# Kernel tuning notes

Hardware: AMD Instinct MI355X
Metric: run time of the kernel (lower is better)

Reference implementation:

```python
import jax, jax.numpy as jnp
import numpy as np

C = 64          # channels
HEADS = 4       # num_heads -> head_dim = 16
HID = int(C * 2.66)  # 170, GDFN hidden channels
B, H, W = 2, 256, 256


def conv1x1(x, w):
    # x: (b,c,h,w), w: (o,c) -> pointwise conv, no bias
    return jnp.einsum('bchw,oc->bohw', x, w)


def dwconv3x3(x, w):
    # depthwise 3x3, SAME padding; w: (C,1,3,3)
    return jax.lax.conv_general_dilated(
        x, w, window_strides=(1, 1), padding='SAME',
        feature_group_count=x.shape[1],
        dimension_numbers=('NCHW', 'OIHW', 'NCHW'))


def layer_norm_c(x, w, b):
    # torch: LayerNorm over channel dim of (b, hw, c), eps=1e-5
    mu = x.mean(axis=1, keepdims=True)
    var = ((x - mu) ** 2).mean(axis=1, keepdims=True)
    xn = (x - mu) / jnp.sqrt(var + 1e-5)
    return xn * w[None, :, None, None] + b[None, :, None, None]


def l2norm(x):
    # F.normalize(dim=-1), eps=1e-12
    n = jnp.sqrt(jnp.sum(x * x, axis=-1, keepdims=True))
    return x / jnp.maximum(n, 1e-12)


def mdta(x, temp, w_qkv, w_qkv_dw, w_po, w_kv, w_kv_dw, w_pof):
    b, c, h, w_ = x.shape
    d = c // HEADS
    qkv = dwconv3x3(conv1x1(x, w_qkv), w_qkv_dw)
    q, k, v = jnp.split(qkv, 3, axis=1)
    rs = lambda t: t.reshape(b, HEADS, d, h * w_)
    q, k, v = l2norm(rs(q)), l2norm(rs(k)), rs(v)
    # channel attention: (b,heads,d,d), softmax over last dim
    attn = jax.nn.softmax(jnp.einsum('bhdn,bhen->bhde', q, k) * temp, axis=-1)
    out = conv1x1(jnp.einsum('bhde,bhen->bhdn', attn, v).reshape(b, c, h, w_), w_po)
    # second gated branch: kv from `out`, reuse attn (qf/kf/attnf are dead code in source)
    kvf = dwconv3x3(conv1x1(out, w_kv), w_kv_dw)
    _kf, vf = jnp.split(kvf, 2, axis=1)
    vf = rs(vf)
    outf = conv1x1(jnp.einsum('bhde,bhen->bhdn', attn, vf).reshape(b, c, h, w_), w_pof)
    return outf


def gdfn(x, w_in, w_dw, w_out):
    x12 = dwconv3x3(conv1x1(x, w_in), w_dw)
    x1, x2 = jnp.split(x12, 2, axis=1)
    return conv1x1(jax.nn.gelu(x1, approximate=False) * x2, w_out)


def setup_inputs() -> dict:
    key = jax.random.key(0)
    ks = jax.random.split(key, 10)
    s = 0.05
    return {
        'x': jax.random.normal(ks[0], (B, C, H, W), jnp.float32),
        'n1_w': jnp.ones((C,), jnp.float32),
        'n1_b': jnp.zeros((C,), jnp.float32),
        'temp': jnp.ones((1, HEADS, 1, 1), jnp.float32),
        'w_qkv': jax.random.normal(ks[1], (3 * C, C), jnp.float32) * s,
        'w_qkv_dw': jax.random.normal(ks[2], (3 * C, 1, 3, 3), jnp.float32) * s,
        'w_po': jax.random.normal(ks[3], (C, C), jnp.float32) * s,
        'w_kv': jax.random.normal(ks[4], (2 * C, C), jnp.float32) * s,
        'w_kv_dw': jax.random.normal(ks[5], (2 * C, 1, 3, 3), jnp.float32) * s,
        'w_pof': jax.random.normal(ks[6], (C, C), jnp.float32) * s,
        'n2_w': jnp.ones((C,), jnp.float32),
        'n2_b': jnp.zeros((C,), jnp.float32),
        'w_in': jax.random.normal(ks[7], (2 * HID, C), jnp.float32) * s,
        'w_dw': jax.random.normal(ks[8], (2 * HID, 1, 3, 3), jnp.float32) * s,
        'w_out': jax.random.normal(ks[9], (C, HID), jnp.float32) * s,
    }


def reference(x, n1_w, n1_b, temp, w_qkv, w_qkv_dw, w_po, w_kv, w_kv_dw, w_pof,
              n2_w, n2_b, w_in, w_dw, w_out):
    x = x + mdta(layer_norm_c(x, n1_w, n1_b), temp,
                 w_qkv, w_qkv_dw, w_po, w_kv, w_kv_dw, w_pof)
    x = x + gdfn(layer_norm_c(x, n2_w, n2_b), w_in, w_dw, w_out)
    return x
```

## Files before the change

### kernel.cpp

```cpp
#include <hip/hip_runtime.h>
#include <hip/hip_bf16.h>
#include <math.h>

#define NPB 65536
#define BATCH 2
#define NTOT (BATCH * NPB)

typedef unsigned short u16;
typedef __attribute__((ext_vector_type(8))) short short8;
typedef __attribute__((ext_vector_type(4))) short short4v;
typedef __attribute__((ext_vector_type(4))) float f32x4;


__device__ __forceinline__ float bf2f(u16 u) {
  union { unsigned u; float f; } v; v.u = ((unsigned)u) << 16; return v.f;
}
__device__ __forceinline__ u16 f2bf(float f) {
  union { float f; unsigned u; } v; v.f = f;
  unsigned r = v.u + 0x7FFFu + ((v.u >> 16) & 1u);
  return (u16)(r >> 16);
}
__device__ __forceinline__ unsigned pk2(float a, float b) {
  return (unsigned)f2bf(a) | ((unsigned)f2bf(b) << 16);
}
__device__ __forceinline__ f32x4 mm(short8 a, short8 b, f32x4 c) {
  return __builtin_amdgcn_mfma_f32_16x16x32_bf16(a, b, c, 0, 0, 0);
}
__device__ __forceinline__ short8 ldfrag(const u16* F, int frag, int l) {
  return *reinterpret_cast<const short8*>(F + ((size_t)frag * 64 + l) * 8);
}
__device__ __forceinline__ void st4(u16* p, f32x4 c) {
  uint2 v; v.x = pk2(c[0], c[1]); v.y = pk2(c[2], c[3]);
  *reinterpret_cast<uint2*>(p) = v;
}
__device__ __forceinline__ float gelu_t(float a) {
  const float z = 0.7978845608f * fmaf(0.044715f * a, a * a, a);
  const float e = __expf(2.f * z);
  const float th = 1.f - 2.f / (e + 1.f);
  return 0.5f * a * (1.f + th);
}

__global__ __launch_bounds__(64) void k_wprep(
    const float* __restrict__ wqkv, const float* __restrict__ win,
    const float* __restrict__ wout, u16* __restrict__ WQf,
    u16* __restrict__ WIf, u16* __restrict__ WOf)
{
  const int f = blockIdx.x;
  const int l = threadIdx.x;
  const int fr = l & 15, fq = l >> 4;
  short8 v;
  u16* dst;
  if (f < 24) {
    const int t = f >> 1, kh = f & 1;
    const int row = t * 16 + fr;
#pragma unroll
    for (int j = 0; j < 8; ++j)
      v[j] = (short)f2bf(wqkv[(size_t)row * 64 + kh * 32 + fq * 8 + j]);
    dst = WQf + ((size_t)f * 64 + l) * 8;
  } else if (f < 68) {
    const int fi = f - 24;
    const int g = fi >> 1, kh = fi & 1;
    const int half = g / 11, t = g % 11;
    const int col = half * 176 + t * 16 + fr;
    const int row = col < 170 ? col : (col < 176 ? -1 : (col < 346 ? col - 6 : -1));
#pragma unroll
    for (int j = 0; j < 8; ++j)
      v[j] = (row < 0) ? (short)0
             : (short)f2bf(win[(size_t)row * 64 + kh * 32 + fq * 8 + j]);
    dst = WIf + ((size_t)fi * 64 + l) * 8;
  } else {
    const int fi = f - 68;
    const int t = fi / 6, kh = fi % 6;
    const int row = t * 16 + fr;
#pragma unroll
    for (int j = 0; j < 8; ++j) {
      const int k = kh * 32 + fq * 8 + j;
      v[j] = (k < 170) ? (short)f2bf(wout[(size_t)row * 170 + k]) : (short)0;
    }
    dst = WOf + ((size_t)fi * 64 + l) * 8;
  }
  *reinterpret_cast<short8*>(dst) = v;
}

__global__ __launch_bounds__(256, 4) void k_ln1(
    const float* __restrict__ x, const float* __restrict__ n1w,
    const float* __restrict__ n1b, u16* __restrict__ Y1)
{
  const int n = blockIdx.x * 256 + threadIdx.x;
  const int b = blockIdx.y;
  const size_t pix = (size_t)b * NPB + n;
  const float* xb = x + ((size_t)b * 64) * NPB + n;
  float y[64];
  float mu = 0.f;
#pragma unroll
  for (int c = 0; c < 64; ++c) { y[c] = xb[(size_t)c * NPB]; mu += y[c]; }
  mu *= (1.f / 64.f);
  float var = 0.f;
#pragma unroll
  for (int c = 0; c < 64; ++c) { float d = y[c] - mu; var = fmaf(d, d, var); }
  const float rstd = rsqrtf(var * (1.f / 64.f) + 1e-5f);
#pragma unroll
  for (int c = 0; c < 64; ++c) y[c] = (y[c] - mu) * rstd * n1w[c] + n1b[c];
#pragma unroll
  for (int cb = 0; cb < 4; ++cb) {
    u16* dst = Y1 + ((size_t)cb * NTOT + pix) * 16;
    uint4 v0, v1;
    v0.x = pk2(y[cb*16+0],  y[cb*16+1]);  v0.y = pk2(y[cb*16+2],  y[cb*16+3]);
    v0.z = pk2(y[cb*16+4],  y[cb*16+5]);  v0.w = pk2(y[cb*16+6],  y[cb*16+7]);
    v1.x = pk2(y[cb*16+8],  y[cb*16+9]);  v1.y = pk2(y[cb*16+10], y[cb*16+11]);
    v1.z = pk2(y[cb*16+12], y[cb*16+13]); v1.w = pk2(y[cb*16+14], y[cb*16+15]);
    *reinterpret_cast<uint4*>(dst) = v0;
    *reinterpret_cast<uint4*>(dst + 8) = v1;
  }
}

__global__ __launch_bounds__(256, 2) void g_qkvp(
    const u16* __restrict__ Y1, const u16* __restrict__ WQf,
    u16* __restrict__ qkvp)
{
  const int l = threadIdx.x & 63, fr = l & 15, fq = l >> 4;
  const int wv = blockIdx.x * 4 + (threadIdx.x >> 6);
  const int nw = gridDim.x * 4;
  short8 A[12][2];
#pragma unroll
  for (int t = 0; t < 12; ++t)
#pragma unroll
    for (int kh = 0; kh < 2; ++kh) A[t][kh] = ldfrag(WQf, t * 2 + kh, l);
  const size_t hof = (size_t)(fq & 1) * 8;
  for (int tile = wv; tile < 8192; tile += nw) {
    const size_t n = (size_t)tile * 16 + fr;
    const short8 b0 = *reinterpret_cast<const short8*>(
        Y1 + (((size_t)(fq >> 1)) * NTOT + n) * 16 + hof);
    const short8 b1 = *reinterpret_cast<const short8*>(
        Y1 + (((size_t)(2 + (fq >> 1))) * NTOT + n) * 16 + hof);
    f32x4 c[12];
#pragma unroll
    for (int t = 0; t < 12; ++t) c[t] = f32x4{0.f, 0.f, 0.f, 0.f};
#pragma unroll
    for (int t = 0; t < 12; ++t) c[t] = mm(A[t][0], b0, c[t]);
#pragma unroll
    for (int t = 0; t < 12; ++t) c[t] = mm(A[t][1], b1, c[t]);
#pragma unroll
    for (int t = 0; t < 12; ++t)
      st4(qkvp + ((size_t)t * NTOT + n) * 16 + fq * 4, c[t]);
  }
}

template<int CH, int STRIP>
__global__ __launch_bounds__(256, 2) void k_dwr(
    const u16* __restrict__ in, u16* __restrict__ out,
    const float* __restrict__ wdw, int wofs)
{
  typedef short __attribute__((ext_vector_type(CH))) shortC;
  constexpr int LPP = 16 / CH;
  constexpr int NX  = 256 / LPP;
  constexpr int XC  = 256 / NX;
  const int t = threadIdx.x;
  const int sub = t % LPP, xi = t / LPP;
  const int q = blockIdx.x / XC, xc = blockIdx.x % XC;
  const int strip = blockIdx.y, b = blockIdx.z;
  const int x = xc * NX + xi;
  const int y0 = strip * STRIP;
  const int e0 = sub * CH;
  const int c0 = q * 16 + e0;

  const u16* pin = in + ((size_t)q * NTOT + (size_t)b * NPB) * 16 + e0;

  float w[9][CH];
#pragma unroll
  for (int ch = 0; ch < CH; ++ch) {
    const int row = wofs + c0 + ch;
#pragma unroll
    for (int tap = 0; tap < 9; ++tap)
      w[tap][ch] = wdw[(size_t)row * 9 + tap];
  }

  auto LD = [&](int yy, int xx) -> shortC {
    shortC v;
#pragma unroll
    for (int j = 0; j < CH; ++j) v[j] = 0;
    if ((unsigned)yy < 256u && (unsigned)xx < 256u)
      v = *reinterpret_cast<const shortC*>(pin + (size_t)(yy * 256 + xx) * 16);
    return v;
  };

  shortC r[3][3];
  r[0][0] = LD(y0 - 1, x - 1); r[0][1] = LD(y0 - 1, x); r[0][2] = LD(y0 - 1, x + 1);
  r[1][0] = LD(y0, x - 1);     r[1][1] = LD(y0, x);     r[1][2] = LD(y0, x + 1);

#pragma unroll 2
  for (int yy = 0; yy < STRIP; ++yy) {
    const int y = y0 + yy;
    r[2][0] = LD(y + 1, x - 1); r[2][1] = LD(y + 1, x); r[2][2] = LD(y + 1, x + 1);
    float acc[CH];
#pragma unroll
    for (int ch = 0; ch < CH; ++ch) acc[ch] = 0.f;
#pragma unroll
    for (int ky = 0; ky < 3; ++ky)
#pragma unroll
      for (int kx = 0; kx < 3; ++kx)
#pragma unroll
        for (int ch = 0; ch < CH; ++ch)
          acc[ch] = fmaf(w[ky * 3 + kx][ch], bf2f((u16)r[ky][kx][ch]), acc[ch]);
    u16* po = out + ((size_t)q * NTOT + (size_t)b * NPB +
                     (size_t)(y * 256 + x)) * 16 + e0;
    uint4 o;
    o.x = pk2(acc[0], acc[1]); o.y = pk2(acc[2], acc[3]);
    o.z = pk2(acc[4], acc[5]); o.w = pk2(acc[6], acc[7]);
    *reinterpret_cast<uint4*>(po) = o;
#pragma unroll
    for (int dx = 0; dx < 3; ++dx) { r[0][dx] = r[1][dx]; r[1][dx] = r[2][dx]; }
  }
}

__global__ __launch_bounds__(256, 2) void g_windwg(
    const u16* __restrict__ Y2, const u16* __restrict__ WIf,
    const float* __restrict__ wdw, u16* __restrict__ Hg)
{
  __shared__ __align__(16) u16 sy[336 * 72];
  __shared__ __align__(16) u16 sh[336 * 36];
  __shared__ __align__(16) u16 swt[2 * 9 * 176];
  const int t = threadIdx.x;
  const int tx0 = blockIdx.x * 16, ty0 = blockIdx.y * 16;
  const int b = blockIdx.z;
  const size_t bofs = (size_t)b * NPB;

  for (int i = t; i < 2 * 9 * 176; i += 256) {
    const int pl = i / (9 * 176);
    const int r = i % (9 * 176);
    const int tap = r / 176, c = r % 176;
    swt[i] = (c < 170) ? f2bf(wdw[((size_t)(pl * 170 + c)) * 9 + tap]) : (u16)0;
  }
  for (int idx = t; idx < 336; idx += 256) {
    const int py = idx / 18, px = idx % 18;
    const int gy = ty0 + py - 1, gx = tx0 + px - 1;
    const bool ok = (idx < 324) && ((unsigned)gy < 256u) && ((unsigned)gx < 256u);
#pragma unroll
    for (int cb = 0; cb < 4; ++cb) {
      short8 v0, v1;
      if (ok) {
        const u16* src = Y2 + ((size_t)cb * NTOT + bofs + (size_t)(gy * 256 + gx)) * 16;
        v0 = *reinterpret_cast<const short8*>(src);
        v1 = *reinterpret_cast<const short8*>(src + 8);
      } else {
#pragma unroll
        for (int j = 0; j < 8; ++j) { v0[j] = 0; v1[j] = 0; }
      }
      *reinterpret_cast<short8*>(&sy[idx * 72 + cb * 16]) = v0;
      *reinterpret_cast<short8*>(&sy[idx * 72 + cb * 16 + 8]) = v1;
    }
  }
  __syncthreads();

  const int w = t >> 6, l = t & 63, fr = l & 15, fq = l >> 4;
  const int sub = t & 3, colx = (t >> 2) & 15, rg = t >> 6;
  const int e0 = sub * 4;

  for (int q = 0; q < 11; ++q) {
    const short8 a10 = ldfrag(WIf, q * 2, l);
    const short8 a11 = ldfrag(WIf, q * 2 + 1, l);
    const short8 a20 = ldfrag(WIf, (11 + q) * 2, l);
    const short8 a21 = ldfrag(WIf, (11 + q) * 2 + 1, l);
    for (int i = w; i < 21; i += 4) {
      const u16* sp = &sy[(i * 16 + fr) * 72];
      const short8 b0 = *reinterpret_cast<const short8*>(sp + fq * 8);
      const short8 b1 = *reinterpret_cast<const short8*>(sp + 32 + fq * 8);
      f32x4 c1 = {0.f, 0.f, 0.f, 0.f}, c2 = {0.f, 0.f, 0.f, 0.f};
      c1 = mm(a10, b0, c1); c1 = mm(a11, b1, c1);
      c2 = mm(a20, b0, c2); c2 = mm(a21, b1, c2);
      u16* dp = &sh[(i * 16 + fr) * 36];
      st4(dp + fq * 4, c1);
      st4(dp + 16 + fq * 4, c2);
    }
    __syncthreads();

    float wf[2][9][4];
#pragma unroll
    for (int pl = 0; pl < 2; ++pl)
#pragma unroll
      for (int tap = 0; tap < 9; ++tap) {
        const short4v wv = *reinterpret_cast<const short4v*>(
            &swt[(pl * 9 + tap) * 176 + q * 16 + e0]);
#pragma unroll
        for (int j = 0; j < 4; ++j) wf[pl][tap][j] = bf2f((u16)wv[j]);
      }
    short4v rwin[3][3][2];
    auto LDR = [&](int hr, int slot) {
#pragma unroll
      for (int dx = 0; dx < 3; ++dx)
#pragma unroll
        for (int pl = 0; pl < 2; ++pl)
          rwin[slot][dx][pl] = *reinterpret_cast<const short4v*>(
              &sh[(hr * 18 + colx + dx) * 36 + pl * 16 + e0]);
    };
    const int r0 = rg * 4;
    LDR(r0, 0); LDR(r0 + 1, 1);
#pragma unroll
    for (int k = 0; k < 4; ++k) {
      LDR(r0 + k + 2, (k + 2) % 3);
      const int s0 = k % 3, s1 = (k + 1) % 3, s2 = (k + 2) % 3;
      float acc[2][4] = {{0.f, 0.f, 0.f, 0.f}, {0.f, 0.f, 0.f, 0.f}};
#pragma unroll
      for (int pl = 0; pl < 2; ++pl)
#pragma unroll
        for (int dx = 0; dx < 3; ++dx)
#pragma unroll
          for (int j = 0; j < 4; ++j) {
            acc[pl][j] = fmaf(wf[pl][0 + dx][j], bf2f((u16)rwin[s0][dx][pl][j]), acc[pl][j]);
            acc[pl][j] = fmaf(wf[pl][3 + dx][j], bf2f((u16)rwin[s1][dx][pl][j]), acc[pl][j]);
            acc[pl][j] = fmaf(wf[pl][6 + dx][j], bf2f((u16)rwin[s2][dx][pl][j]), acc[pl][j]);
          }
      float v[4];
#pragma unroll
      for (int j = 0; j < 4; ++j) v[j] = gelu_t(acc[0][j]) * acc[1][j];
      const int gy = ty0 + r0 + k, gx = tx0 + colx;
      uint2 o; o.x = pk2(v[0], v[1]); o.y = pk2(v[2], v[3]);
      *reinterpret_cast<uint2*>(
          Hg + ((size_t)q * NTOT + bofs + (size_t)(gy * 256 + gx)) * 16 + e0) = o;
    }
    __syncthreads();
  }
}

__global__ __launch_bounds__(256, 2) void k_gram_p(
    const u16* __restrict__ qkv, float* __restrict__ part)
{
  __shared__ __align__(16) u16 lds[32][520];
  const int chunk = blockIdx.x, h = blockIdx.y, b = blockIdx.z;
  const int t = threadIdx.x;
#pragma unroll
  for (int i = 0; i < 2; ++i) {
    const int p = t + i * 256;
    const size_t pix = (size_t)b * NPB + chunk * 512 + p;
    const u16* srcq = qkv + ((size_t)h * NTOT + pix) * 16;
    const u16* srck = qkv + ((size_t)(4 + h) * NTOT + pix) * 16;
    const short8 q0 = *reinterpret_cast<const short8*>(srcq);
    const short8 q1 = *reinterpret_cast<const short8*>(srcq + 8);
    const short8 k0 = *reinterpret_cast<const short8*>(srck);
    const short8 k1 = *reinterpret_cast<const short8*>(srck + 8);
#pragma unroll
    for (int j = 0; j < 8; ++j) {
      lds[j][p] = (u16)q0[j];  lds[8 + j][p] = (u16)q1[j];
      lds[16 + j][p] = (u16)k0[j]; lds[24 + j][p] = (u16)k1[j];
    }
  }
  __syncthreads();
  const int w = t >> 6, l = t & 63, fr = l & 15, fq = l >> 4;
  if (w >= 3) return;
  float* pp = part + ((size_t)((b * 4 + h) * 128) + chunk) * 288;
  const int rowA = (w == 2) ? 16 + fr : fr;
  const int rowB = (w == 0) ? 16 + fr : rowA;
  f32x4 acc = {0.f, 0.f, 0.f, 0.f};
#pragma unroll
  for (int kt = 0; kt < 16; ++kt) {
    const short8 a  = *reinterpret_cast<const short8*>(&lds[rowA][kt * 32 + fq * 8]);
    const short8 bb = *reinterpret_cast<const short8*>(&lds[rowB][kt * 32 + fq * 8]);
    acc = mm(a, bb, acc);
  }
  if (w == 0) {
#pragma unroll
    for (int r = 0; r < 4; ++r) pp[(fq * 4 + r) * 16 + fr] = acc[r];
  } else if ((fr >> 2) == fq) {
    pp[(w == 1 ? 256 : 272) + fr] = acc[fr & 3];
  }
}

__global__ __launch_bounds__(320) void k_gram_red(
    const float* __restrict__ part, float* __restrict__ G,
    float* __restrict__ Sq, float* __restrict__ Sk)
{
  const int bh = blockIdx.x;
  const int t = threadIdx.x;
  if (t >= 288) return;
  const float* p = part + (size_t)bh * 128 * 288 + t;
  float s = 0.f;
  for (int ch = 0; ch < 128; ++ch) s += p[(size_t)ch * 288];
  const int b = bh >> 2, h = bh & 3;
  if (t < 256) G[bh * 256 + t] = s;
  else if (t < 272) Sq[b * 64 + h * 16 + (t - 256)] = s;
  else Sk[b * 64 + h * 16 + (t - 272)] = s;
}

__global__ __launch_bounds__(256) void k_attn(
    const float* __restrict__ G, const float* __restrict__ Sq,
    const float* __restrict__ Sk, const float* __restrict__ temp,
    const float* __restrict__ wpo, const float* __restrict__ wkv,
    const float* __restrict__ wpof, u16* __restrict__ Pf,
    u16* __restrict__ M2f)
{
  __shared__ float attn[BATCH][4][16][16];
  __shared__ float M1[BATCH][64][64];
  __shared__ float rq[128], rk[128];
  const int t = threadIdx.x;
  if (t < 128) {
    rq[t] = 1.f / fmaxf(sqrtf(Sq[t]), 1e-12f);
    rk[t] = 1.f / fmaxf(sqrtf(Sk[t]), 1e-12f);
  }
  __syncthreads();
  if (t < 128) {
    const int b = t >> 6, h = (t >> 4) & 3, d = t & 15;
    const float tm = temp[h];
    const float* g = G + ((b * 4 + h) * 16 + d) * 16;
    const float rqd = rq[b * 64 + h * 16 + d];
    float L[16], mx = -1e30f;
#pragma unroll
    for (int e = 0; e < 16; ++e) {
      L[e] = g[e] * rqd * rk[b * 64 + h * 16 + e] * tm;
      mx = fmaxf(mx, L[e]);
    }
    float s = 0.f;
#pragma unroll
    for (int e = 0; e < 16; ++e) { L[e] = expf(L[e] - mx); s += L[e]; }
    const float inv = 1.f / s;
#pragma unroll
    for (int e = 0; e < 16; ++e) attn[b][h][d][e] = L[e] * inv;
  }
  __syncthreads();
  for (int s0 = 0; s0 < 32; ++s0) {
    const int idx = t * 32 + s0;
    const int b = idx >> 12, o = (idx >> 6) & 63, c = idx & 63;
    const int h = c >> 4, e = c & 15;
    float a = 0.f;
#pragma unroll
    for (int d = 0; d < 16; ++d) a = fmaf(wpo[o * 64 + h * 16 + d], attn[b][h][d][e], a);
    M1[b][o][c] = a;
  }
  __syncthreads();
  for (int it = 0; it < 4; ++it) {
    const int idx = it * 256 + t;
    const int l = idx & 63;
    const int fi = idx >> 6;
    const int b = fi >> 3, tt = (fi >> 1) & 3, kh = fi & 1;
    const int fr = l & 15, fq = l >> 4;
    const int o = tt * 16 + fr;
    short8 pv, mv;
#pragma unroll
    for (int j = 0; j < 8; ++j) {
      const int c = kh * 32 + fq * 8 + j;
      const int h = c >> 4, e = c & 15;
      float a2 = 0.f;
#pragma unroll
      for (int d = 0; d < 16; ++d)
        a2 = fmaf(wpof[o * 64 + h * 16 + d], attn[b][h][d][e], a2);
      mv[j] = (short)f2bf(a2);
      float a = 0.f;
      for (int jj = 0; jj < 64; ++jj)
        a = fmaf(wkv[(64 + o) * 64 + jj], M1[b][jj][c], a);
      pv[j] = (short)f2bf(a);
    }
    *reinterpret_cast<short8*>(Pf + ((size_t)fi * 64 + l) * 8) = pv;
    *reinterpret_cast<short8*>(M2f + ((size_t)fi * 64 + l) * 8) = mv;
  }
}

__global__ __launch_bounds__(256, 2) void g_pv(
    const u16* __restrict__ qkv, const u16* __restrict__ Pf,
    u16* __restrict__ vfp)
{
  const int l = threadIdx.x & 63, fr = l & 15, fq = l >> 4;
  const int wv = blockIdx.x * 4 + (threadIdx.x >> 6);
  const int nw = gridDim.x * 4;
  const int b = blockIdx.z;
  short8 A[4][2];
#pragma unroll
  for (int t = 0; t < 4; ++t)
#pragma unroll
    for (int kh = 0; kh < 2; ++kh)
      A[t][kh] = ldfrag(Pf, (b * 4 + t) * 2 + kh, l);
  const size_t hof = (size_t)(fq & 1) * 8;
  for (int tile = wv; tile < 4096; tile += nw) {
    const size_t n = (size_t)b * NPB + (size_t)tile * 16 + fr;
    const short8 b0 = *reinterpret_cast<const short8*>(
        qkv + ((size_t)(8 + (fq >> 1)) * NTOT + n) * 16 + hof);
    const short8 b1 = *reinterpret_cast<const short8*>(
        qkv + ((size_t)(10 + (fq >> 1)) * NTOT + n) * 16 + hof);
    f32x4 c[4];
#pragma unroll
    for (int t = 0; t < 4; ++t) c[t] = f32x4{0.f, 0.f, 0.f, 0.f};
#pragma unroll
    for (int t = 0; t < 4; ++t) c[t] = mm(A[t][0], b0, c[t]);
#pragma unroll
    for (int t = 0; t < 4; ++t) c[t] = mm(A[t][1], b1, c[t]);
#pragma unroll
    for (int t = 0; t < 4; ++t)
      st4(vfp + ((size_t)t * NTOT + n) * 16 + fq * 4, c[t]);
  }
}

__global__ __launch_bounds__(256, 2) void g_x2ln(
    const u16* __restrict__ vf, const u16* __restrict__ M2f,
    const float* __restrict__ x, const float* __restrict__ n2w,
    const float* __restrict__ n2b, u16* __restrict__ X2,
    u16* __restrict__ Y2)
{
  const int l = threadIdx.x & 63, fr = l & 15, fq = l >> 4;
  const int wv = blockIdx.x * 4 + (threadIdx.x >> 6);
  const int nw = gridDim.x * 4;
  const int b = blockIdx.z;
  short8 A[4][2];
#pragma unroll
  for (int t = 0; t < 4; ++t)
#pragma unroll
    for (int kh = 0; kh < 2; ++kh)
      A[t][kh] = ldfrag(M2f, (b * 4 + t) * 2 + kh, l);
  const size_t hof = (size_t)(fq & 1) * 8;
  for (int tile = wv; tile < 4096; tile += nw) {
    const int pix0 = tile * 16;
    const size_t n = (size_t)b * NPB + pix0 + fr;
    const short8 b0 = *reinterpret_cast<const short8*>(
        vf + ((size_t)(fq >> 1) * NTOT + n) * 16 + hof);
    const short8 b1 = *reinterpret_cast<const short8*>(
        vf + ((size_t)(2 + (fq >> 1)) * NTOT + n) * 16 + hof);
    f32x4 c[4];
#pragma unroll
    for (int t = 0; t < 4; ++t) c[t] = f32x4{0.f, 0.f, 0.f, 0.f};
#pragma unroll
    for (int t = 0; t < 4; ++t) c[t] = mm(A[t][0], b0, c[t]);
#pragma unroll
    for (int t = 0; t < 4; ++t) c[t] = mm(A[t][1], b1, c[t]);
    const int pix = pix0 + fr;
#pragma unroll
    for (int t = 0; t < 4; ++t)
#pragma unroll
      for (int r = 0; r < 4; ++r)
        c[t][r] += x[((size_t)(b * 64 + t * 16 + fq * 4 + r)) * NPB + pix];
#pragma unroll
    for (int t = 0; t < 4; ++t)
      st4(X2 + ((size_t)t * NTOT + n) * 16 + fq * 4, c[t]);
    float s = 0.f;
#pragma unroll
    for (int t = 0; t < 4; ++t)
#pragma unroll
      for (int r = 0; r < 4; ++r) s += c[t][r];
    s += __shfl_xor(s, 16); s += __shfl_xor(s, 32);
    const float mu = s * (1.f / 64.f);
    float ss = 0.f;
#pragma unroll
    for (int t = 0; t < 4; ++t)
#pragma unroll
      for (int r = 0; r < 4; ++r) { float d = c[t][r] - mu; ss = fmaf(d, d, ss); }
    ss += __shfl_xor(ss, 16); ss += __shfl_xor(ss, 32);
    const float rstd = rsqrtf(ss * (1.f / 64.f) + 1e-5f);
#pragma unroll
    for (int t = 0; t < 4; ++t)
#pragma unroll
      for (int r = 0; r < 4; ++r) {
        const int oc = t * 16 + fq * 4 + r;
        c[t][r] = (c[t][r] - mu) * rstd * n2w[oc] + n2b[oc];
      }
#pragma unroll
    for (int t = 0; t < 4; ++t)
      st4(Y2 + ((size_t)t * NTOT + n) * 16 + fq * 4, c[t]);
  }
}

__global__ __launch_bounds__(256, 2) void g_out(
    const u16* __restrict__ hg, const u16* __restrict__ WOf,
    const u16* __restrict__ X2, float* __restrict__ out)
{
  const int l = threadIdx.x & 63, fr = l & 15, fq = l >> 4;
  const int wv = blockIdx.x * 4 + (threadIdx.x >> 6);
  const int nw = gridDim.x * 4;
  short8 A[4][6];
#pragma unroll
  for (int t = 0; t < 4; ++t)
#pragma unroll
    for (int kh = 0; kh < 6; ++kh)
      A[t][kh] = ldfrag(WOf, t * 6 + kh, l);
  const size_t hof = (size_t)(fq & 1) * 8;
  for (int tile = wv; tile < 8192; tile += nw) {
    const size_t n = (size_t)tile * 16 + fr;
    short8 bb[6];
#pragma unroll
    for (int kh = 0; kh < 6; ++kh) {
      int hb = kh * 2 + (fq >> 1);
      if (hb > 10) hb = 10;
      bb[kh] = *reinterpret_cast<const short8*>(
          hg + ((size_t)hb * NTOT + n) * 16 + hof);
    }
    f32x4 c[4];
#pragma unroll
    for (int t = 0; t < 4; ++t) c[t] = f32x4{0.f, 0.f, 0.f, 0.f};
#pragma unroll
    for (int kh = 0; kh < 6; ++kh)
#pragma unroll
      for (int t = 0; t < 4; ++t) c[t] = mm(A[t][kh], bb[kh], c[t]);
    const int b = (int)(n >> 16);
    const int pix = (int)(n & 65535);
#pragma unroll
    for (int t = 0; t < 4; ++t) {
      const uint2 xv = *reinterpret_cast<const uint2*>(
          X2 + ((size_t)t * NTOT + n) * 16 + fq * 4);
      const u16 h0 = (u16)(xv.x & 0xffff), h1 = (u16)(xv.x >> 16);
      const u16 h2 = (u16)(xv.y & 0xffff), h3 = (u16)(xv.y >> 16);
      const int ocb = b * 64 + t * 16 + fq * 4;
      out[((size_t)(ocb + 0)) * NPB + pix] = c[t][0] + bf2f(h0);
      out[((size_t)(ocb + 1)) * NPB + pix] = c[t][1] + bf2f(h1);
      out[((size_t)(ocb + 2)) * NPB + pix] = c[t][2] + bf2f(h2);
      out[((size_t)(ocb + 3)) * NPB + pix] = c[t][3] + bf2f(h3);
    }
  }
}

extern "C" void kernel_launch(void* const* d_in, const int* in_sizes, int n_in,
                              void* d_out, int out_size, void* d_ws, size_t ws_size,
                              hipStream_t stream)
{
  const float* x     = (const float*)d_in[0];
  const float* n1w   = (const float*)d_in[1];
  const float* n1b   = (const float*)d_in[2];
  const float* temp  = (const float*)d_in[3];
  const float* wqkv  = (const float*)d_in[4];
  const float* wqkvd = (const float*)d_in[5];
  const float* wpo   = (const float*)d_in[6];
  const float* wkv   = (const float*)d_in[7];
  const float* wkvd  = (const float*)d_in[8];
  const float* wpof  = (const float*)d_in[9];
  const float* n2w   = (const float*)d_in[10];
  const float* n2b   = (const float*)d_in[11];
  const float* win   = (const float*)d_in[12];
  const float* wdw   = (const float*)d_in[13];
  const float* wout  = (const float*)d_in[14];
  float* out = (float*)d_out;

  char* ws = (char*)d_ws;
  const size_t offA  = 0;
  const size_t offB  = 16777216;
  const size_t offC  = offB + 50331648;
  const size_t offHg = offC + 50331648;
  const size_t offX2 = offHg + 46137344 + 256;
  const size_t offSm = offX2 + 16777216;

  u16* Y1   = (u16*)(ws + offA);
  u16* VFP  = (u16*)(ws + offA);
  u16* Y2   = (u16*)(ws + offA);
  u16* QKVp = (u16*)(ws + offB);
  u16* VF   = (u16*)(ws + offB);
  u16* QKV  = (u16*)(ws + offC);
  u16* Hg   = (u16*)(ws + offHg);
  u16* X2   = (u16*)(ws + offX2);
  float* part = (float*)(ws + offSm);
  float* G    = (float*)(ws + offSm + 1179648);
  float* Sq   = (float*)(ws + offSm + 1179648 + 8192);
  float* Sk   = (float*)(ws + offSm + 1179648 + 8704);
  u16* Pf     = (u16*)(ws + offSm + 1179648 + 9216);
  u16* M2f    = (u16*)(ws + offSm + 1179648 + 25600);
  u16* WQf    = (u16*)(ws + offSm + 1179648 + 41984);
  u16* WIf    = (u16*)(ws + offSm + 1179648 + 66560);
  u16* WOf    = (u16*)(ws + offSm + 1179648 + 111616);

  k_wprep<<<dim3(92), 64, 0, stream>>>(wqkv, win, wout, WQf, WIf, WOf);
  k_ln1<<<dim3(NPB / 256, BATCH), 256, 0, stream>>>(x, n1w, n1b, Y1);
  g_qkvp<<<dim3(512), 256, 0, stream>>>(Y1, WQf, QKVp);
  k_dwr<8, 16><<<dim3(24, 16, BATCH), 256, 0, stream>>>(QKVp, QKV, wqkvd, 0);
  k_gram_p<<<dim3(128, 4, BATCH), 256, 0, stream>>>(QKV, part);
  k_gram_red<<<dim3(BATCH * 4), 320, 0, stream>>>(part, G, Sq, Sk);
  k_attn<<<dim3(1), 256, 0, stream>>>(G, Sq, Sk, temp, wpo, wkv, wpof, Pf, M2f);
  g_pv<<<dim3(256, 1, BATCH), 256, 0, stream>>>(QKV, Pf, VFP);
  k_dwr<8, 8><<<dim3(8, 32, BATCH), 256, 0, stream>>>(VFP, VF, wkvd, 64);
  g_x2ln<<<dim3(256, 1, BATCH), 256, 0, stream>>>(VF, M2f, x, n2w, n2b, X2, Y2);
  g_windwg<<<dim3(16, 16, BATCH), 256, 0, stream>>>(Y2, WIf, wdw, Hg);
  g_out<<<dim3(512), 256, 0, stream>>>(Hg, WOf, X2, out);
}
```

Before: 232.5 us.

## Pad Y2 with zero border and read MFMA operands directly from global in GDFN

g_x2ln now writes Y2 into a zero-padded 258x258 layout, and a small kernel zeroes the border. g_windwg no longer stages the input halo in shared memory; it loads MFMA B fragments straight from the padded global buffer. The tile height drops from 16 to 8 rows, which doubles the grid and cuts shared memory, and the sh row stride changes to 38 to reduce bank conflicts. This removes the LDS staging pass and the boundary branches, and should raise occupancy. In exchange, halo rows are recomputed more often (180 of 128 pixels instead of 324 of 256), and global loads now happen inside the q loop, so they are repeated 11 times per block.

Measured after the change: 257.0 us. +10.5%, slower.

```diff
diff --git a/kernel.cpp b/kernel.cpp
--- a/kernel.cpp
+++ b/kernel.cpp
@@ -5,6 +5,8 @@
 #define NPB 65536
 #define BATCH 2
 #define NTOT (BATCH * NPB)
+#define NPP 66564
+#define NTOTP (BATCH * NPP)
 
 typedef unsigned short u16;
 typedef __attribute__((ext_vector_type(8))) short short8;
@@ -80,6 +82,23 @@
     dst = WOf + ((size_t)fi * 64 + l) * 8;
   }
   *reinterpret_cast<short8*>(dst) = v;
+}
+
+__global__ __launch_bounds__(256) void k_zb(u16* __restrict__ Y2P)
+{
+  const int cb = blockIdx.x >> 1, b = blockIdx.x & 1;
+  const int t = threadIdx.x;
+  for (int i = t; i < 1028; i += 256) {
+    int y, x;
+    if (i < 258) { y = 0; x = i; }
+    else if (i < 516) { y = 257; x = i - 258; }
+    else if (i < 772) { y = i - 515; x = 0; }
+    else { y = i - 771; x = 257; }
+    u16* p = Y2P + ((size_t)cb * NTOTP + (size_t)b * NPP + (size_t)(y * 258 + x)) * 16;
+    uint4 z = {0, 0, 0, 0};
+    *reinterpret_cast<uint4*>(p) = z;
+    *reinterpret_cast<uint4*>(p + 8) = z;
+  }
 }
 
 __global__ __launch_bounds__(256, 4) void k_ln1(
@@ -214,16 +233,16 @@
 }
 
 __global__ __launch_bounds__(256, 2) void g_windwg(
-    const u16* __restrict__ Y2, const u16* __restrict__ WIf,
+    const u16* __restrict__ Y2P, const u16* __restrict__ WIf,
     const float* __restrict__ wdw, u16* __restrict__ Hg)
 {
-  __shared__ __align__(16) u16 sy[336 * 72];
-  __shared__ __align__(16) u16 sh[336 * 36];
+  __shared__ __align__(16) u16 sh[192 * 38];
   __shared__ __align__(16) u16 swt[2 * 9 * 176];
   const int t = threadIdx.x;
-  const int tx0 = blockIdx.x * 16, ty0 = blockIdx.y * 16;
+  const int tx0 = blockIdx.x * 16, ty0 = blockIdx.y * 8;
   const int b = blockIdx.z;
   const size_t bofs = (size_t)b * NPB;
+  const size_t bofsP = (size_t)b * NPP;
 
   for (int i = t; i < 2 * 9 * 176; i += 256) {
     const int pl = i / (9 * 176);
@@ -231,44 +250,33 @@
     const int tap = r / 176, c = r % 176;
     swt[i] = (c < 170) ? f2bf(wdw[((size_t)(pl * 170 + c)) * 9 + tap]) : (u16)0;
   }
-  for (int idx = t; idx < 336; idx += 256) {
-    const int py = idx / 18, px = idx % 18;
-    const int gy = ty0 + py - 1, gx = tx0 + px - 1;
-    const bool ok = (idx < 324) && ((unsigned)gy < 256u) && ((unsigned)gx < 256u);
-#pragma unroll
-    for (int cb = 0; cb < 4; ++cb) {
-      short8 v0, v1;
-      if (ok) {
-        const u16* src = Y2 + ((size_t)cb * NTOT + bofs + (size_t)(gy * 256 + gx)) * 16;
-        v0 = *reinterpret_cast<const short8*>(src);
-        v1 = *reinterpret_cast<const short8*>(src + 8);
-      } else {
-#pragma unroll
-        for (int j = 0; j < 8; ++j) { v0[j] = 0; v1[j] = 0; }
-      }
-      *reinterpret_cast<short8*>(&sy[idx * 72 + cb * 16]) = v0;
-      *reinterpret_cast<short8*>(&sy[idx * 72 + cb * 16 + 8]) = v1;
-    }
-  }
   __syncthreads();
 
   const int w = t >> 6, l = t & 63, fr = l & 15, fq = l >> 4;
   const int sub = t & 3, colx = (t >> 2) & 15, rg = t >> 6;
   const int e0 = sub * 4;
+  const size_t hof = (size_t)(fq & 1) * 8;
+  const size_t cb0 = (size_t)(fq >> 1) * NTOTP;
+  const size_t cb1 = (size_t)(2 + (fq >> 1)) * NTOTP;
 
   for (int q = 0; q < 11; ++q) {
     const short8 a10 = ldfrag(WIf, q * 2, l);
     const short8 a11 = ldfrag(WIf, q * 2 + 1, l);
     const short8 a20 = ldfrag(WIf, (11 + q) * 2, l);
     const short8 a21 = ldfrag(WIf, (11 + q) * 2 + 1, l);
-    for (int i = w; i < 21; i += 4) {
-      const u16* sp = &sy[(i * 16 + fr) * 72];
-      const short8 b0 = *reinterpret_cast<const short8*>(sp + fq * 8);
-      const short8 b1 = *reinterpret_cast<const short8*>(sp + 32 + fq * 8);
+    for (int i = w; i < 12; i += 4) {
+      const int hidx = i * 16 + fr;
+      const int hs = hidx < 179 ? hidx : 179;
+      const int py = hs / 18, px = hs % 18;
+      const size_t ppix = bofsP + (size_t)((ty0 + py) * 258 + tx0 + px);
+      const short8 b0 = *reinterpret_cast<const short8*>(
+          Y2P + (cb0 + ppix) * 16 + hof);
+      const short8 b1 = *reinterpret_cast<const short8*>(
+          Y2P + (cb1 + ppix) * 16 + hof);
       f32x4 c1 = {0.f, 0.f, 0.f, 0.f}, c2 = {0.f, 0.f, 0.f, 0.f};
       c1 = mm(a10, b0, c1); c1 = mm(a11, b1, c1);
       c2 = mm(a20, b0, c2); c2 = mm(a21, b1, c2);
-      u16* dp = &sh[(i * 16 + fr) * 36];
+      u16* dp = &sh[hidx * 38];
       st4(dp + fq * 4, c1);
       st4(dp + 16 + fq * 4, c2);
     }
@@ -291,12 +299,12 @@
 #pragma unroll
         for (int pl = 0; pl < 2; ++pl)
           rwin[slot][dx][pl] = *reinterpret_cast<const short4v*>(
-              &sh[(hr * 18 + colx + dx) * 36 + pl * 16 + e0]);
+              &sh[(hr * 18 + colx + dx) * 38 + pl * 16 + e0]);
     };
-    const int r0 = rg * 4;
+    const int r0 = rg * 2;
     LDR(r0, 0); LDR(r0 + 1, 1);
 #pragma unroll
-    for (int k = 0; k < 4; ++k) {
+    for (int k = 0; k < 2; ++k) {
       LDR(r0 + k + 2, (k + 2) % 3);
       const int s0 = k % 3, s1 = (k + 1) % 3, s2 = (k + 2) % 3;
       float acc[2][4] = {{0.f, 0.f, 0.f, 0.f}, {0.f, 0.f, 0.f, 0.f}};
@@ -491,7 +499,7 @@
     const u16* __restrict__ vf, const u16* __restrict__ M2f,
     const float* __restrict__ x, const float* __restrict__ n2w,
     const float* __restrict__ n2b, u16* __restrict__ X2,
-    u16* __restrict__ Y2)
+    u16* __restrict__ Y2P)
 {
   const int l = threadIdx.x & 63, fr = l & 15, fq = l >> 4;
   const int wv = blockIdx.x * 4 + (threadIdx.x >> 6);
@@ -548,9 +556,11 @@
         const int oc = t * 16 + fq * 4 + r;
         c[t][r] = (c[t][r] - mu) * rstd * n2w[oc] + n2b[oc];
       }
+    const int yy = pix >> 8, xx = pix & 255;
+    const size_t ppix = (size_t)b * NPP + (size_t)((yy + 1) * 258 + xx + 1);
 #pragma unroll
     for (int t = 0; t < 4; ++t)
-      st4(Y2 + ((size_t)t * NTOT + n) * 16 + fq * 4, c[t]);
+      st4(Y2P + ((size_t)t * NTOTP + ppix) * 16 + fq * 4, c[t]);
   }
 }
 
@@ -625,7 +635,7 @@
 
   char* ws = (char*)d_ws;
   const size_t offA  = 0;
-  const size_t offB  = 16777216;
+  const size_t offB  = 17301504;
   const size_t offC  = offB + 50331648;
   const size_t offHg = offC + 50331648;
   const size_t offX2 = offHg + 46137344 + 256;
@@ -633,7 +643,7 @@
 
   u16* Y1   = (u16*)(ws + offA);
   u16* VFP  = (u16*)(ws + offA);
-  u16* Y2   = (u16*)(ws + offA);
+  u16* Y2P  = (u16*)(ws + offA);
   u16* QKVp = (u16*)(ws + offB);
   u16* VF   = (u16*)(ws + offB);
   u16* QKV  = (u16*)(ws + offC);
@@ -658,7 +668,8 @@
   k_attn<<<dim3(1), 256, 0, stream>>>(G, Sq, Sk, temp, wpo, wkv, wpof, Pf, M2f);
   g_pv<<<dim3(256, 1, BATCH), 256, 0, stream>>>(QKV, Pf, VFP);
   k_dwr<8, 8><<<dim3(8, 32, BATCH), 256, 0, stream>>>(VFP, VF, wkvd, 64);
-  g_x2ln<<<dim3(256, 1, BATCH), 256, 0, stream>>>(VF, M2f, x, n2w, n2b, X2, Y2);
-  g_windwg<<<dim3(16, 16, BATCH), 256, 0, stream>>>(Y2, WIf, wdw, Hg);
+  k_zb<<<dim3(8), 256, 0, stream>>>(Y2P);
+  g_x2ln<<<dim3(256, 1, BATCH), 256, 0, stream>>>(VF, M2f, x, n2w, n2b, X2, Y2P);
+  g_windwg<<<dim3(16, 32, BATCH), 256, 0, stream>>>(Y2P, WIf, wdw, Hg);
   g_out<<<dim3(512), 256, 0, stream>>>(Hg, WOf, X2, out);
 }
```
